# Kernel tuning notes

Measured on AMD Instinct MI355X. Metric: run time of the kernel, lower is better.

## Reference

```python
import jax, jax.numpy as jnp
import numpy as np

N_USER, N_VIDEO, N_PUB, N_TAG = 200000, 100000, 20000, 5000
EMB = 128
HALF = EMB // 2
LAYER_NUM = 3


def setup_inputs() -> dict:
    key = jax.random.key(0)
    ks = jax.random.split(key, 20)
    inp = {
        "user_emb": jax.random.normal(ks[0], (N_USER, EMB), jnp.float32),
        "video_emb": jax.random.normal(ks[1], (N_VIDEO, EMB), jnp.float32),
        "publisher_emb": jax.random.normal(ks[2], (N_PUB, EMB), jnp.float32),
        "tag_emb": jax.random.normal(ks[3], (N_TAG, EMB), jnp.float32),
    }
    # (name, E, n_src, n_dst)
    rels = [
        ("uv", 1500000, N_USER, N_VIDEO),
        ("vu", 1500000, N_VIDEO, N_USER),
        ("up", 800000, N_USER, N_PUB),
        ("pu", 800000, N_PUB, N_USER),
        ("vt", 800000, N_VIDEO, N_TAG),
        ("tv", 800000, N_TAG, N_VIDEO),
        ("pt", 400000, N_PUB, N_TAG),
        ("tp", 400000, N_TAG, N_PUB),
    ]
    for i, (name, E, ns, nd) in enumerate(rels):
        inp[name + "_src"] = jax.random.randint(ks[4 + 2 * i], (E,), 0, ns, jnp.int32)
        inp[name + "_dst"] = jax.random.randint(ks[5 + 2 * i], (E,), 0, nd, jnp.int32)
    return inp


def _seg_mean(feat, src, dst, num_dst):
    # copy_u + mean: gather half-dim src features, segment-mean onto dst.
    msg = feat[src]                                             # [E, HALF]
    s = jax.ops.segment_sum(msg, dst, num_segments=num_dst)     # [num_dst, HALF]
    deg = jax.ops.segment_sum(jnp.ones_like(dst, dtype=feat.dtype), dst,
                              num_segments=num_dst)
    return s / jnp.maximum(deg, 1.0)[:, None]  # zero-in-degree nodes -> 0 (DGL behavior)


def reference(user_emb, video_emb, publisher_emb, tag_emb,
              uv_src, uv_dst, vu_src, vu_dst,
              up_src, up_dst, pu_src, pu_dst,
              vt_src, vt_dst, tv_src, tv_dst,
              pt_src, pt_dst, tp_src, tp_dst):

    def layer(u, v, p, t):
        # user dst: [vu, pu]; video dst: [uv, tv]; publisher dst: [up, tp]; tag dst: [vt, pt]
        vu = _seg_mean(v[:, :HALF], vu_src, vu_dst, N_USER)
        pu = _seg_mean(p[:, :HALF], pu_src, pu_dst, N_USER)
        uv = _seg_mean(u[:, :HALF], uv_src, uv_dst, N_VIDEO)
        tv = _seg_mean(t[:, :HALF], tv_src, tv_dst, N_VIDEO)
        up = _seg_mean(u[:, HALF:], up_src, up_dst, N_PUB)
        tp = _seg_mean(t[:, HALF:], tp_src, tp_dst, N_PUB)
        vt = _seg_mean(v[:, HALF:], vt_src, vt_dst, N_TAG)
        pt = _seg_mean(p[:, HALF:], pt_src, pt_dst, N_TAG)
        return (jnp.concatenate([vu, pu], axis=1),
                jnp.concatenate([uv, tv], axis=1),
                jnp.concatenate([up, tp], axis=1),
                jnp.concatenate([vt, pt], axis=1))

    pu_, pv_, pp_, pt_ = user_emb, video_emb, publisher_emb, tag_emb
    u, v, p, t = user_emb, video_emb, publisher_emb, tag_emb
    for i in range(LAYER_NUM):
        u, v, p, t = layer(u, v, p, t)
        w = 1.0 / (i + 2)
        pu_ = pu_ + u * w
        pv_ = pv_ + v * w
        pp_ = pp_ + p * w
        pt_ = pt_ + t * w
    return (pu_, pv_, pp_, pt_)
```

## Files before the change

### kernel.cpp

```cpp
#include <hip/hip_runtime.h>
#include <stdint.h>

#define EMB 128
#define PCAP 12288
#define SCAP 13312

static constexpr int N_USER = 200000, N_VIDEO = 100000, N_PUB = 20000, N_TAG = 5000;
static constexpr int ROW_U = 0, ROW_V = 200000, ROW_P = 300000, ROW_T = 320000;
static constexpr int ROWS = 325000;
static constexpr int TOTAL_E = 7000000;
static constexpr int TOTAL_GROUPS = 650000;
static constexpr int TILE = 8192;
static constexpr int SORT_MAX = TOTAL_E + 7 * TOTAL_GROUPS;

using f32x4 = __attribute__((ext_vector_type(4))) float;
using u32x4 = __attribute__((ext_vector_type(4))) unsigned int;
using u32x2 = __attribute__((ext_vector_type(2))) unsigned int;

__device__ inline unsigned bf16_rne(float f) {
  unsigned u = __float_as_uint(f);
  return (u + 0x7fffu + ((u >> 16) & 1u)) >> 16;
}
__device__ inline unsigned pack_bf16x2(float lo, float hi) {
  return bf16_rne(lo) | (bf16_rne(hi) << 16);
}

__device__ inline unsigned fp8enc(float f) {
  unsigned b = __float_as_uint(f);
  unsigned s = (b >> 24) & 0x80u;
  unsigned ae = b & 0x7FFFFFFFu;
  unsigned r = ae + 0x7FFFFu + ((ae >> 20) & 1u);
  unsigned e = r >> 23;
  if (e < 121u) {
    float av = __uint_as_float(ae);
    unsigned m = (unsigned)__builtin_rintf(av * 512.0f);
    return s | m;
  }
  return s | ((e - 120u) << 3) | ((r >> 20) & 7u);
}
#if __has_builtin(__builtin_amdgcn_cvt_f32_fp8)
#define DEC4(w, x0, x1, x2, x3) \
  x0 += __builtin_amdgcn_cvt_f32_fp8((int)(w), 0); \
  x1 += __builtin_amdgcn_cvt_f32_fp8((int)(w), 1); \
  x2 += __builtin_amdgcn_cvt_f32_fp8((int)(w), 2); \
  x3 += __builtin_amdgcn_cvt_f32_fp8((int)(w), 3);
#else
__device__ inline float fp8dec(unsigned b) {
  unsigned s = (b & 0x80u) << 24;
  unsigned e = (b >> 3) & 0xFu;
  unsigned m = b & 7u;
  if (e == 0) { float f = (float)m * 0.001953125f; return s ? -f : f; }
  return __uint_as_float(s | ((e + 120u) << 23) | (m << 20));
}
#define DEC4(w, x0, x1, x2, x3) \
  x0 += fp8dec((w) & 0xffu); x1 += fp8dec(((w) >> 8) & 0xffu); \
  x2 += fp8dec(((w) >> 16) & 0xffu); x3 += fp8dec(((w) >> 24) & 0xffu);
#endif

struct SortDesc {
  int tcum[9];
  int bcum[9];
  int gcum[8];
  int E[8];
  int n_dst[8];
  int wshift[8];
  int zrow[8];
  const int* esrc[8];
  const int* edst[8];
};

struct AggrDesc {
  int cum[9];
  int src_base[8];
  int src_col[8];
  int dst_base[8];
  int dst_col[8];
  const float* demb[8];
};

__global__ __launch_bounds__(256) void part_kernel(SortDesc d, unsigned* __restrict__ pairs,
                                                   int* __restrict__ cursors) {
  __shared__ int cnt[256];
  __shared__ int lcur[256];
  int blk = blockIdx.x;
  int r = 0;
#pragma unroll
  for (int k = 1; k < 8; ++k) if (blk >= d.tcum[k]) r = k;
  int base = (blk - d.tcum[r]) * TILE;
  int n = min(TILE, d.E[r] - base);
  const int* __restrict__ esrc = d.esrc[r];
  const int* __restrict__ edst = d.edst[r];
  int tid = threadIdx.x;
  int B = d.bcum[r + 1] - d.bcum[r];
  int sh = d.wshift[r];
  int msk = (1 << sh) - 1;
  int bb = d.bcum[r];
  if (tid < B) cnt[tid] = 0;
  __syncthreads();
  for (int i = tid; i < n; i += 256)
    atomicAdd(&cnt[edst[base + i] >> sh], 1);
  __syncthreads();
  if (tid < B) {
    int c = cnt[tid];
    lcur[tid] = c ? atomicAdd(&cursors[bb + tid], c) : 0;
  }
  __syncthreads();
  for (int i = tid; i < n; i += 256) {
    int dv = edst[base + i];
    int sv = esrc[base + i];
    int b = dv >> sh;
    int pos = atomicAdd(&lcur[b], 1);
    if (pos < PCAP)
      pairs[(size_t)(bb + b) * PCAP + pos] = ((unsigned)(dv & msk) << 18) | (unsigned)sv;
  }
}

__global__ __launch_bounds__(256) void build_kernel(SortDesc d, const unsigned* __restrict__ pairs,
                                                    const int* __restrict__ cursors,
                                                    int* __restrict__ gcounter,
                                                    int* __restrict__ sorted,
                                                    int* __restrict__ Beg, int* __restrict__ Deg) {
  __shared__ int cnt[1024];
  __shared__ int poff[1025];
  __shared__ int stage[SCAP];
  __shared__ int wsums[4];
  __shared__ int sh_gbase;
  int bucket = blockIdx.x;
  int r = 0;
#pragma unroll
  for (int k = 1; k < 8; ++k) if (bucket >= d.bcum[k]) r = k;
  int bl = bucket - d.bcum[r];
  int sh = d.wshift[r];
  int first = bl << sh;
  int Wa = min(1 << sh, d.n_dst[r] - first);
  int zr = d.zrow[r];
  int tid = threadIdx.x;
  int n_b = min(cursors[bucket], PCAP);
  const unsigned* __restrict__ bp = pairs + (size_t)bucket * PCAP;

  for (int i = tid; i < 1024; i += 256) cnt[i] = 0;
  __syncthreads();
  for (int i = tid; i < n_b; i += 256)
    atomicAdd(&cnt[bp[i] >> 18], 1);
  __syncthreads();

  int t4 = tid * 4;
  int c0 = cnt[t4], c1 = cnt[t4 + 1], c2 = cnt[t4 + 2], c3 = cnt[t4 + 3];
  int p0 = (c0 + 7) & ~7, p1 = (c1 + 7) & ~7, p2 = (c2 + 7) & ~7, p3 = (c3 + 7) & ~7;
  int s = p0 + p1 + p2 + p3;
  int lane = tid & 63, wv = tid >> 6;
  int v = s;
#pragma unroll
  for (int dd = 1; dd < 64; dd <<= 1) {
    int t = __shfl_up(v, dd);
    if (lane >= dd) v += t;
  }
  if (lane == 63) wsums[wv] = v;
  __syncthreads();
  if (tid == 0) {
    int run = 0;
#pragma unroll
    for (int k = 0; k < 4; ++k) { int t = wsums[k]; wsums[k] = run; run += t; }
  }
  __syncthreads();
  int ex = wsums[wv] + (v - s);
  if (tid == 255) {
    int tot = ex + s;
    sh_gbase = atomicAdd(gcounter, tot);
    poff[1024] = min(tot, SCAP);
  }
  __syncthreads();
  int gbase = sh_gbase;
  int o0 = ex, o1 = ex + p0, o2 = o1 + p1, o3 = o2 + p2;
  cnt[t4] = o0; cnt[t4 + 1] = o1; cnt[t4 + 2] = o2; cnt[t4 + 3] = o3;
  poff[t4] = o0; poff[t4 + 1] = o1; poff[t4 + 2] = o2; poff[t4 + 3] = o3;
  int g0 = d.gcum[r] + first + t4;
  if (t4 + 0 < Wa) { Beg[g0 + 0] = gbase + o0; Deg[g0 + 0] = c0; }
  if (t4 + 1 < Wa) { Beg[g0 + 1] = gbase + o1; Deg[g0 + 1] = c1; }
  if (t4 + 2 < Wa) { Beg[g0 + 2] = gbase + o2; Deg[g0 + 2] = c2; }
  if (t4 + 3 < Wa) { Beg[g0 + 3] = gbase + o3; Deg[g0 + 3] = c3; }
  __syncthreads();

  for (int i = tid; i < n_b; i += 256) {
    unsigned pr = bp[i];
    int pos = atomicAdd(&cnt[pr >> 18], 1);
    if (pos < SCAP) stage[pos] = (int)(pr & 0x3FFFFu);
  }
  __syncthreads();
#pragma unroll
  for (int jj = 0; jj < 4; ++jj) {
    int j = t4 + jj;
    int end_ = min((j < 1023) ? poff[j + 1] : poff[1024], SCAP);
    for (int k = cnt[j]; k < end_; ++k) stage[k] = zr;
  }
  __syncthreads();

  int tot = poff[1024];
  for (int i = tid; i < tot; i += 256)
    sorted[gbase + i] = stage[i];
}

__global__ void convert_kernel(const float* __restrict__ u, const float* __restrict__ v,
                               const float* __restrict__ p, const float* __restrict__ t,
                               uint16_t* __restrict__ featA, uint16_t* __restrict__ featB,
                               unsigned char* __restrict__ f1f8) {
  int idx = blockIdx.x * blockDim.x + threadIdx.x;
  const int total8 = (ROWS + 1) * EMB / 8;
  if (idx >= total8) return;
  int flat = idx * 8;
  int row = flat >> 7;
  if (row == ROWS) {
    uint4 z = {0u, 0u, 0u, 0u};
    *(uint4*)(featA + flat) = z;
    *(uint4*)(featB + flat) = z;
    if (f1f8) { uint2 z2 = {0u, 0u}; *(uint2*)(f1f8 + flat) = z2; }
    return;
  }
  int col = flat & 127;
  const float* s;
  if (row < ROW_V)      s = u + (size_t)row * EMB + col;
  else if (row < ROW_P) s = v + (size_t)(row - ROW_V) * EMB + col;
  else if (row < ROW_T) s = p + (size_t)(row - ROW_P) * EMB + col;
  else                  s = t + (size_t)(row - ROW_T) * EMB + col;
  float4 f0 = *(const float4*)s;
  float4 f1 = *((const float4*)s + 1);
  uint4 o;
  o.x = pack_bf16x2(f0.x, f0.y);
  o.y = pack_bf16x2(f0.z, f0.w);
  o.z = pack_bf16x2(f1.x, f1.y);
  o.w = pack_bf16x2(f1.z, f1.w);
  *(uint4*)(featA + flat) = o;
}

#define ACC(q) \
  a0 += __uint_as_float((q).x << 16); a1 += __uint_as_float((q).x & 0xffff0000u); \
  a2 += __uint_as_float((q).y << 16); a3 += __uint_as_float((q).y & 0xffff0000u); \
  a4 += __uint_as_float((q).z << 16); a5 += __uint_as_float((q).z & 0xffff0000u); \
  a6 += __uint_as_float((q).w << 16); a7 += __uint_as_float((q).w & 0xffff0000u);

#define ACC8(qq) \
  DEC4((qq).x, a0, a1, a2, a3); DEC4((qq).y, a4, a5, a6, a7);

template<int M>
__global__ __launch_bounds__(256) void aggr_kernel(AggrDesc d,
    const uint16_t* __restrict__ gsrc_bf, const unsigned char* __restrict__ gsrc_f8,
    uint16_t* __restrict__ dst_bf, unsigned char* __restrict__ dst_f8,
    const uint16_t* __restrict__ f1_bf, const uint16_t* __restrict__ demb_bf,
    float* __restrict__ out,
    const int* __restrict__ sorted, const int* __restrict__ Beg,
    const int* __restrict__ Deg) {
  if ((M == 1 || M == 3) && blockIdx.x == 0 && threadIdx.x < 16) {
    uint2 z = {0u, 0u};
    *(uint2*)(dst_f8 + (size_t)ROWS * EMB + threadIdx.x * 8) = z;
  }
  int g = blockIdx.x * 32 + (threadIdx.x >> 3);
  if (g >= TOTAL_GROUPS) return;
  int lane = threadIdx.x & 7;
  int r = 0;
#pragma unroll
  for (int k = 1; k < 8; ++k) if (g >= d.cum[k]) r = k;
  int n = g - d.cum[r];
  int beg = Beg[g], dg = Deg[g];
  float recip = 1.0f / (float)(dg > 0 ? dg : 1);
  constexpr bool GB = (M == 0 || M == 3 || M == 4);
  const uint16_t* __restrict__ sb16 =
      GB ? gsrc_bf + (size_t)d.src_base[r] * EMB + d.src_col[r] + lane * 8 : nullptr;
  const unsigned char* __restrict__ sb8 =
      !GB ? gsrc_f8 + (size_t)d.src_base[r] * EMB + d.src_col[r] + lane * 8 : nullptr;
  float a0 = 0.f, a1 = 0.f, a2 = 0.f, a3 = 0.f, a4 = 0.f, a5 = 0.f, a6 = 0.f, a7 = 0.f;
  int nchunk = (dg + 7) >> 3;
  const int* ep = sorted + beg;
  int4 iA0 = {0,0,0,0}, iA1 = {0,0,0,0};
  if (nchunk > 0) { iA0 = *(const int4*)ep; iA1 = *(const int4*)(ep + 4); }
  for (int c = 0; c < nchunk; ++c) {
    int4 iB0 = {0,0,0,0}, iB1 = {0,0,0,0};
    if (c + 1 < nchunk) { iB0 = *(const int4*)(ep + 8); iB1 = *(const int4*)(ep + 12); }
    if (GB) {
      uint4 q0 = *(const uint4*)(sb16 + (size_t)iA0.x * EMB);
      uint4 q1 = *(const uint4*)(sb16 + (size_t)iA0.y * EMB);
      uint4 q2 = *(const uint4*)(sb16 + (size_t)iA0.z * EMB);
      uint4 q3 = *(const uint4*)(sb16 + (size_t)iA0.w * EMB);
      uint4 q4 = *(const uint4*)(sb16 + (size_t)iA1.x * EMB);
      uint4 q5 = *(const uint4*)(sb16 + (size_t)iA1.y * EMB);
      uint4 q6 = *(const uint4*)(sb16 + (size_t)iA1.z * EMB);
      uint4 q7 = *(const uint4*)(sb16 + (size_t)iA1.w * EMB);
      __builtin_amdgcn_sched_barrier(0);
      ACC(q0); ACC(q1); ACC(q2); ACC(q3);
      ACC(q4); ACC(q5); ACC(q6); ACC(q7);
    } else {
      uint2 q0 = *(const uint2*)(sb8 + (size_t)iA0.x * EMB);
      uint2 q1 = *(const uint2*)(sb8 + (size_t)iA0.y * EMB);
      uint2 q2 = *(const uint2*)(sb8 + (size_t)iA0.z * EMB);
      uint2 q3 = *(const uint2*)(sb8 + (size_t)iA0.w * EMB);
      uint2 q4 = *(const uint2*)(sb8 + (size_t)iA1.x * EMB);
      uint2 q5 = *(const uint2*)(sb8 + (size_t)iA1.y * EMB);
      uint2 q6 = *(const uint2*)(sb8 + (size_t)iA1.z * EMB);
      uint2 q7 = *(const uint2*)(sb8 + (size_t)iA1.w * EMB);
      __builtin_amdgcn_sched_barrier(0);
      ACC8(q0); ACC8(q1); ACC8(q2); ACC8(q3);
      ACC8(q4); ACC8(q5); ACC8(q6); ACC8(q7);
    }
    iA0 = iB0; iA1 = iB1; ep += 8;
  }
  a0 *= recip; a1 *= recip; a2 *= recip; a3 *= recip;
  a4 *= recip; a5 *= recip; a6 *= recip; a7 *= recip;

  int col = d.dst_col[r] + lane * 8;
  size_t dpos = (size_t)(d.dst_base[r] + n) * EMB + col;

  if (M == 0 || M == 4) {
    u32x4 ov;
    ov.x = pack_bf16x2(a0, a1);
    ov.y = pack_bf16x2(a2, a3);
    ov.z = pack_bf16x2(a4, a5);
    ov.w = pack_bf16x2(a6, a7);
    __builtin_nontemporal_store(ov, (u32x4*)(dst_bf + dpos));
    if (M == 4) {
      u32x2 o8;
      o8.x = fp8enc(a0) | (fp8enc(a1) << 8) | (fp8enc(a2) << 16) | (fp8enc(a3) << 24);
      o8.y = fp8enc(a4) | (fp8enc(a5) << 8) | (fp8enc(a6) << 16) | (fp8enc(a7) << 24);
      __builtin_nontemporal_store(o8, (u32x2*)(dst_f8 + dpos));
    }
    return;
  }
  if (M == 1 || M == 3) {
    u32x2 ov;
    ov.x = fp8enc(a0) | (fp8enc(a1) << 8) | (fp8enc(a2) << 16) | (fp8enc(a3) << 24);
    ov.y = fp8enc(a4) | (fp8enc(a5) << 8) | (fp8enc(a6) << 16) | (fp8enc(a7) << 24);
    __builtin_nontemporal_store(ov, (u32x2*)(dst_f8 + dpos));
    return;
  }

  u32x4 q1 = __builtin_nontemporal_load((const u32x4*)(f1_bf + dpos));
  u32x2 qf = __builtin_nontemporal_load((const u32x2*)(gsrc_f8 + dpos));
  float g0 = 0.f, g1 = 0.f, g2 = 0.f, g3 = 0.f, g4 = 0.f, g5 = 0.f, g6 = 0.f, g7 = 0.f;
  DEC4(qf.x, g0, g1, g2, g3);
  DEC4(qf.y, g4, g5, g6, g7);
  f32x4 v0, v1;
  if (demb_bf) {
    u32x4 qe = __builtin_nontemporal_load((const u32x4*)(demb_bf + dpos));
    v0.x = __uint_as_float(qe.x << 16); v0.y = __uint_as_float(qe.x & 0xffff0000u);
    v0.z = __uint_as_float(qe.y << 16); v0.w = __uint_as_float(qe.y & 0xffff0000u);
    v1.x = __uint_as_float(qe.z << 16); v1.y = __uint_as_float(qe.z & 0xffff0000u);
    v1.z = __uint_as_float(qe.w << 16); v1.w = __uint_as_float(qe.w & 0xffff0000u);
  } else {
    const f32x4* de = (const f32x4*)(d.demb[r] + (size_t)n * EMB + col);
    v0 = __builtin_nontemporal_load(de);
    v1 = __builtin_nontemporal_load(de + 1);
  }
  const float w1 = 0.5f, w2 = 1.0f / 3.0f, w3 = 0.25f;
  v0.x += w1 * __uint_as_float(q1.x << 16)         + w2 * g0 + w3 * a0;
  v0.y += w1 * __uint_as_float(q1.x & 0xffff0000u) + w2 * g1 + w3 * a1;
  v0.z += w1 * __uint_as_float(q1.y << 16)         + w2 * g2 + w3 * a2;
  v0.w += w1 * __uint_as_float(q1.y & 0xffff0000u) + w2 * g3 + w3 * a3;
  v1.x += w1 * __uint_as_float(q1.z << 16)         + w2 * g4 + w3 * a4;
  v1.y += w1 * __uint_as_float(q1.z & 0xffff0000u) + w2 * g5 + w3 * a5;
  v1.z += w1 * __uint_as_float(q1.w << 16)         + w2 * g6 + w3 * a6;
  v1.w += w1 * __uint_as_float(q1.w & 0xffff0000u) + w2 * g7 + w3 * a7;
  __builtin_nontemporal_store(v0, (f32x4*)(out + dpos));
  __builtin_nontemporal_store(v1, (f32x4*)(out + dpos) + 1);
}

extern "C" void kernel_launch(void* const* d_in, const int* in_sizes, int n_in,
                              void* d_out, int out_size, void* d_ws, size_t ws_size,
                              hipStream_t stream) {
  const float* emb_u = (const float*)d_in[0];
  const float* emb_v = (const float*)d_in[1];
  const float* emb_p = (const float*)d_in[2];
  const float* emb_t = (const float*)d_in[3];

  struct RelInfo { int si, di, E, n_dst, src_base, src_col, dst_base, dst_col, wshift; };
  const RelInfo rels[8] = {
    {12, 13,  800000, N_TAG,   ROW_V, 64, ROW_T,  0,  5},
    {16, 17,  400000, N_TAG,   ROW_P, 64, ROW_T, 64,  5},
    { 8,  9,  800000, N_PUB,   ROW_U, 64, ROW_P,  0,  7},
    {18, 19,  400000, N_PUB,   ROW_T, 64, ROW_P, 64,  7},
    { 4,  5, 1500000, N_VIDEO, ROW_U,  0, ROW_V,  0,  9},
    {14, 15,  800000, N_VIDEO, ROW_T,  0, ROW_V, 64,  9},
    { 6,  7, 1500000, N_USER,  ROW_V,  0, ROW_U,  0, 10},
    {10, 11,  800000, N_USER,  ROW_P,  0, ROW_U, 64, 10},
  };
  const float* dembs[8] = {emb_t, emb_t, emb_p, emb_p, emb_v, emb_v, emb_u, emb_u};

  char* ws = (char*)d_ws;
  size_t cursor = 0;
  auto take = [&](size_t bytes) -> char* {
    char* p = ws + cursor;
    cursor = (cursor + bytes + 255) & ~(size_t)255;
    return p;
  };
  uint16_t* featA = (uint16_t*)take((size_t)(ROWS + 1) * EMB * 2);
  uint16_t* featB = (uint16_t*)take((size_t)(ROWS + 1) * EMB * 2);
  int* sorted = (int*)take((size_t)SORT_MAX * 4);
  int* Beg    = (int*)take((size_t)TOTAL_GROUPS * 4);
  int* Deg    = (int*)take((size_t)TOTAL_GROUPS * 4);
  unsigned* pairs = (unsigned*)d_ws;

  SortDesc sd;
  AggrDesc ad;
  int tacc = 0, bacc = 0, gacc = 0;
  for (int r = 0; r < 8; ++r) {
    int n_dst = rels[r].n_dst;
    sd.tcum[r] = tacc; tacc += (rels[r].E + TILE - 1) / TILE;
    sd.bcum[r] = bacc; bacc += (n_dst + (1 << rels[r].wshift) - 1) >> rels[r].wshift;
    sd.gcum[r] = gacc;
    sd.E[r] = rels[r].E;
    sd.n_dst[r] = n_dst;
    sd.wshift[r] = rels[r].wshift;
    sd.zrow[r] = ROWS - rels[r].src_base;
    sd.esrc[r] = (const int*)d_in[rels[r].si];
    sd.edst[r] = (const int*)d_in[rels[r].di];

    ad.cum[r] = gacc;
    ad.src_base[r] = rels[r].src_base;
    ad.src_col[r] = rels[r].src_col;
    ad.dst_base[r] = rels[r].dst_base;
    ad.dst_col[r] = rels[r].dst_col;
    ad.demb[r] = dembs[r];
    gacc += n_dst;
  }
  sd.tcum[8] = tacc;
  sd.bcum[8] = bacc;
  ad.cum[8] = gacc;

  int* cursors  = (int*)take((size_t)bacc * 4 + 4);
  int* gcounter = cursors + bacc;

  const size_t f8bytes = (size_t)(ROWS + 1) * EMB;
  size_t base_need = cursor;
  unsigned char* f1fp8 = nullptr;
  unsigned char* f2fp8 = (unsigned char*)featA;
  bool use_fp8_l1 = false;
  const uint16_t* demb_bf = nullptr;
  if (ws_size >= base_need + f8bytes + 256) {
    f1fp8 = (unsigned char*)take(f8bytes);
    use_fp8_l1 = true;
    if (ws_size >= cursor + f8bytes + 256) {
      f2fp8 = (unsigned char*)take(f8bytes);
      demb_bf = featA;
    }
  }

  hipMemsetAsync(cursors, 0, (size_t)(bacc + 1) * 4, stream);
  part_kernel<<<tacc, 256, 0, stream>>>(sd, pairs, cursors);
  build_kernel<<<bacc, 256, 0, stream>>>(sd, pairs, cursors, gcounter, sorted, Beg, Deg);

  convert_kernel<<<((ROWS + 1) * EMB / 8 + 255) / 256, 256, 0, stream>>>(
      emb_u, emb_v, emb_p, emb_t, featA, featB, f1fp8);

  float* out = (float*)d_out;
  const int aggr_blocks = (TOTAL_GROUPS + 31) / 32;
  if (use_fp8_l1) {
    aggr_kernel<4><<<aggr_blocks, 256, 0, stream>>>(ad, featA, nullptr, featB, f1fp8,
                                                    nullptr, nullptr, nullptr, sorted, Beg, Deg);
    aggr_kernel<1><<<aggr_blocks, 256, 0, stream>>>(ad, nullptr, f1fp8, nullptr, f2fp8,
                                                    nullptr, nullptr, nullptr, sorted, Beg, Deg);
  } else {
    aggr_kernel<0><<<aggr_blocks, 256, 0, stream>>>(ad, featA, nullptr, featB, nullptr,
                                                    nullptr, nullptr, nullptr, sorted, Beg, Deg);
    aggr_kernel<3><<<aggr_blocks, 256, 0, stream>>>(ad, featB, nullptr, nullptr, f2fp8,
                                                    nullptr, nullptr, nullptr, sorted, Beg, Deg);
  }
  aggr_kernel<2><<<aggr_blocks, 256, 0, stream>>>(ad, nullptr, f2fp8, nullptr, nullptr,
                                                  featB, demb_bf, out, sorted, Beg, Deg);
}
```

Before: 599.6 us.

## Sub-sort edges by source tile, pad segments to 4, add 4-edge tail path

The build kernel now bins each destination's edges by source-row tile (32K rows), so the gathers for a segment walk source rows in roughly ascending order. The intent is better cache locality in the aggregation gathers. Segment padding drops from 8 to 4, which cuts the number of dummy zero-row gathers. The aggregation loop gains a 4-edge tail step and loads indices with nontemporal loads. In exchange the histogram and scan in the build kernel grow to up to 4096 bins, with a serial per-thread scan over the tiles.

```diff
diff --git a/kernel.cpp b/kernel.cpp
--- a/kernel.cpp
+++ b/kernel.cpp
@@ -4,6 +4,7 @@
 #define EMB 128
 #define PCAP 12288
 #define SCAP 13312
+#define TSHIFT 15
 
 static constexpr int N_USER = 200000, N_VIDEO = 100000, N_PUB = 20000, N_TAG = 5000;
 static constexpr int ROW_U = 0, ROW_V = 200000, ROW_P = 300000, ROW_T = 320000;
@@ -16,6 +17,7 @@
 using f32x4 = __attribute__((ext_vector_type(4))) float;
 using u32x4 = __attribute__((ext_vector_type(4))) unsigned int;
 using u32x2 = __attribute__((ext_vector_type(2))) unsigned int;
+using i32x4 = __attribute__((ext_vector_type(4))) int;
 
 __device__ inline unsigned bf16_rne(float f) {
   unsigned u = __float_as_uint(f);
@@ -64,6 +66,7 @@
   int E[8];
   int n_dst[8];
   int wshift[8];
+  int ntile[8];
   int zrow[8];
   const int* esrc[8];
   const int* edst[8];
@@ -120,34 +123,46 @@
                                                     int* __restrict__ gcounter,
                                                     int* __restrict__ sorted,
                                                     int* __restrict__ Beg, int* __restrict__ Deg) {
-  __shared__ int cnt[1024];
-  __shared__ int poff[1025];
+  __shared__ int bins[4096];
   __shared__ int stage[SCAP];
   __shared__ int wsums[4];
-  __shared__ int sh_gbase;
+  __shared__ int sh_gbase, sh_tot;
   int bucket = blockIdx.x;
   int r = 0;
 #pragma unroll
   for (int k = 1; k < 8; ++k) if (bucket >= d.bcum[k]) r = k;
   int bl = bucket - d.bcum[r];
   int sh = d.wshift[r];
+  int T = d.ntile[r];
   int first = bl << sh;
-  int Wa = min(1 << sh, d.n_dst[r] - first);
+  int W = 1 << sh;
+  int Wa = min(W, d.n_dst[r] - first);
   int zr = d.zrow[r];
   int tid = threadIdx.x;
   int n_b = min(cursors[bucket], PCAP);
   const unsigned* __restrict__ bp = pairs + (size_t)bucket * PCAP;
 
-  for (int i = tid; i < 1024; i += 256) cnt[i] = 0;
-  __syncthreads();
-  for (int i = tid; i < n_b; i += 256)
-    atomicAdd(&cnt[bp[i] >> 18], 1);
+  int NB = W * T;
+  for (int i = tid; i < NB; i += 256) bins[i] = 0;
+  __syncthreads();
+  for (int i = tid; i < n_b; i += 256) {
+    unsigned pr = bp[i];
+    atomicAdd(&bins[(int)(pr >> 18) * T + (int)((pr & 0x3FFFFu) >> TSHIFT)], 1);
+  }
   __syncthreads();
 
   int t4 = tid * 4;
-  int c0 = cnt[t4], c1 = cnt[t4 + 1], c2 = cnt[t4 + 2], c3 = cnt[t4 + 3];
-  int p0 = (c0 + 7) & ~7, p1 = (c1 + 7) & ~7, p2 = (c2 + 7) & ~7, p3 = (c3 + 7) & ~7;
-  int s = p0 + p1 + p2 + p3;
+  int c[4], p[4];
+  int s = 0;
+#pragma unroll
+  for (int jj = 0; jj < 4; ++jj) {
+    int cj = 0;
+    if (t4 + jj < W)
+      for (int t = 0; t < T; ++t) cj += bins[(t4 + jj) * T + t];
+    c[jj] = cj;
+    p[jj] = (cj + 3) & ~3;
+    s += p[jj];
+  }
   int lane = tid & 63, wv = tid >> 6;
   int v = s;
 #pragma unroll
@@ -167,35 +182,50 @@
   if (tid == 255) {
     int tot = ex + s;
     sh_gbase = atomicAdd(gcounter, tot);
-    poff[1024] = min(tot, SCAP);
+    sh_tot = min(tot, SCAP);
   }
   __syncthreads();
   int gbase = sh_gbase;
-  int o0 = ex, o1 = ex + p0, o2 = o1 + p1, o3 = o2 + p2;
-  cnt[t4] = o0; cnt[t4 + 1] = o1; cnt[t4 + 2] = o2; cnt[t4 + 3] = o3;
-  poff[t4] = o0; poff[t4 + 1] = o1; poff[t4 + 2] = o2; poff[t4 + 3] = o3;
-  int g0 = d.gcum[r] + first + t4;
-  if (t4 + 0 < Wa) { Beg[g0 + 0] = gbase + o0; Deg[g0 + 0] = c0; }
-  if (t4 + 1 < Wa) { Beg[g0 + 1] = gbase + o1; Deg[g0 + 1] = c1; }
-  if (t4 + 2 < Wa) { Beg[g0 + 2] = gbase + o2; Deg[g0 + 2] = c2; }
-  if (t4 + 3 < Wa) { Beg[g0 + 3] = gbase + o3; Deg[g0 + 3] = c3; }
+
+  int o[4];
+  {
+    int run = ex;
+#pragma unroll
+    for (int jj = 0; jj < 4; ++jj) { o[jj] = run; run += p[jj]; }
+  }
+#pragma unroll
+  for (int jj = 0; jj < 4; ++jj) {
+    int j = t4 + jj;
+    if (j < W) {
+      int run = o[jj];
+      for (int t = 0; t < T; ++t) {
+        int tmp = bins[j * T + t];
+        bins[j * T + t] = run;
+        run += tmp;
+      }
+      if (j < Wa) {
+        Beg[d.gcum[r] + first + j] = gbase + o[jj];
+        Deg[d.gcum[r] + first + j] = c[jj];
+      }
+    }
+  }
   __syncthreads();
 
   for (int i = tid; i < n_b; i += 256) {
     unsigned pr = bp[i];
-    int pos = atomicAdd(&cnt[pr >> 18], 1);
-    if (pos < SCAP) stage[pos] = (int)(pr & 0x3FFFFu);
+    int sv = (int)(pr & 0x3FFFFu);
+    int pos = atomicAdd(&bins[(int)(pr >> 18) * T + (sv >> TSHIFT)], 1);
+    if (pos < SCAP) stage[pos] = sv;
   }
   __syncthreads();
 #pragma unroll
   for (int jj = 0; jj < 4; ++jj) {
-    int j = t4 + jj;
-    int end_ = min((j < 1023) ? poff[j + 1] : poff[1024], SCAP);
-    for (int k = cnt[j]; k < end_; ++k) stage[k] = zr;
-  }
-  __syncthreads();
-
-  int tot = poff[1024];
+    int end_ = min(o[jj] + p[jj], SCAP);
+    for (int k = o[jj] + c[jj]; k < end_; ++k) stage[k] = zr;
+  }
+  __syncthreads();
+
+  int tot = sh_tot;
   for (int i = tid; i < tot; i += 256)
     sorted[gbase + i] = stage[i];
 }
@@ -268,39 +298,65 @@
   const unsigned char* __restrict__ sb8 =
       !GB ? gsrc_f8 + (size_t)d.src_base[r] * EMB + d.src_col[r] + lane * 8 : nullptr;
   float a0 = 0.f, a1 = 0.f, a2 = 0.f, a3 = 0.f, a4 = 0.f, a5 = 0.f, a6 = 0.f, a7 = 0.f;
-  int nchunk = (dg + 7) >> 3;
+  int P = (dg + 3) & ~3;
+  int n8 = P >> 3;
+  int has4 = P & 4;
   const int* ep = sorted + beg;
-  int4 iA0 = {0,0,0,0}, iA1 = {0,0,0,0};
-  if (nchunk > 0) { iA0 = *(const int4*)ep; iA1 = *(const int4*)(ep + 4); }
-  for (int c = 0; c < nchunk; ++c) {
-    int4 iB0 = {0,0,0,0}, iB1 = {0,0,0,0};
-    if (c + 1 < nchunk) { iB0 = *(const int4*)(ep + 8); iB1 = *(const int4*)(ep + 12); }
+  i32x4 iA0 = {0,0,0,0}, iA1 = {0,0,0,0};
+  if (n8 > 0) {
+    iA0 = __builtin_nontemporal_load((const i32x4*)ep);
+    iA1 = __builtin_nontemporal_load((const i32x4*)ep + 1);
+  }
+  for (int cch = 0; cch < n8; ++cch) {
+    i32x4 iB0 = {0,0,0,0}, iB1 = {0,0,0,0};
+    if (cch + 1 < n8) {
+      iB0 = __builtin_nontemporal_load((const i32x4*)(ep + 8));
+      iB1 = __builtin_nontemporal_load((const i32x4*)(ep + 8) + 1);
+    }
     if (GB) {
-      uint4 q0 = *(const uint4*)(sb16 + (size_t)iA0.x * EMB);
-      uint4 q1 = *(const uint4*)(sb16 + (size_t)iA0.y * EMB);
-      uint4 q2 = *(const uint4*)(sb16 + (size_t)iA0.z * EMB);
-      uint4 q3 = *(const uint4*)(sb16 + (size_t)iA0.w * EMB);
-      uint4 q4 = *(const uint4*)(sb16 + (size_t)iA1.x * EMB);
-      uint4 q5 = *(const uint4*)(sb16 + (size_t)iA1.y * EMB);
-      uint4 q6 = *(const uint4*)(sb16 + (size_t)iA1.z * EMB);
-      uint4 q7 = *(const uint4*)(sb16 + (size_t)iA1.w * EMB);
+      uint4 q0 = *(const uint4*)(sb16 + (size_t)iA0[0] * EMB);
+      uint4 q1 = *(const uint4*)(sb16 + (size_t)iA0[1] * EMB);
+      uint4 q2 = *(const uint4*)(sb16 + (size_t)iA0[2] * EMB);
+      uint4 q3 = *(const uint4*)(sb16 + (size_t)iA0[3] * EMB);
+      uint4 q4 = *(const uint4*)(sb16 + (size_t)iA1[0] * EMB);
+      uint4 q5 = *(const uint4*)(sb16 + (size_t)iA1[1] * EMB);
+      uint4 q6 = *(const uint4*)(sb16 + (size_t)iA1[2] * EMB);
+      uint4 q7 = *(const uint4*)(sb16 + (size_t)iA1[3] * EMB);
       __builtin_amdgcn_sched_barrier(0);
       ACC(q0); ACC(q1); ACC(q2); ACC(q3);
       ACC(q4); ACC(q5); ACC(q6); ACC(q7);
     } else {
-      uint2 q0 = *(const uint2*)(sb8 + (size_t)iA0.x * EMB);
-      uint2 q1 = *(const uint2*)(sb8 + (size_t)iA0.y * EMB);
-      uint2 q2 = *(const uint2*)(sb8 + (size_t)iA0.z * EMB);
-      uint2 q3 = *(const uint2*)(sb8 + (size_t)iA0.w * EMB);
-      uint2 q4 = *(const uint2*)(sb8 + (size_t)iA1.x * EMB);
-      uint2 q5 = *(const uint2*)(sb8 + (size_t)iA1.y * EMB);
-      uint2 q6 = *(const uint2*)(sb8 + (size_t)iA1.z * EMB);
-      uint2 q7 = *(const uint2*)(sb8 + (size_t)iA1.w * EMB);
+      uint2 q0 = *(const uint2*)(sb8 + (size_t)iA0[0] * EMB);
+      uint2 q1 = *(const uint2*)(sb8 + (size_t)iA0[1] * EMB);
+      uint2 q2 = *(const uint2*)(sb8 + (size_t)iA0[2] * EMB);
+      uint2 q3 = *(const uint2*)(sb8 + (size_t)iA0[3] * EMB);
+      uint2 q4 = *(const uint2*)(sb8 + (size_t)iA1[0] * EMB);
+      uint2 q5 = *(const uint2*)(sb8 + (size_t)iA1[1] * EMB);
+      uint2 q6 = *(const uint2*)(sb8 + (size_t)iA1[2] * EMB);
+      uint2 q7 = *(const uint2*)(sb8 + (size_t)iA1[3] * EMB);
       __builtin_amdgcn_sched_barrier(0);
       ACC8(q0); ACC8(q1); ACC8(q2); ACC8(q3);
       ACC8(q4); ACC8(q5); ACC8(q6); ACC8(q7);
     }
     iA0 = iB0; iA1 = iB1; ep += 8;
+  }
+  if (has4) {
+    i32x4 i0 = __builtin_nontemporal_load((const i32x4*)ep);
+    if (GB) {
+      uint4 q0 = *(const uint4*)(sb16 + (size_t)i0[0] * EMB);
+      uint4 q1 = *(const uint4*)(sb16 + (size_t)i0[1] * EMB);
+      uint4 q2 = *(const uint4*)(sb16 + (size_t)i0[2] * EMB);
+      uint4 q3 = *(const uint4*)(sb16 + (size_t)i0[3] * EMB);
+      __builtin_amdgcn_sched_barrier(0);
+      ACC(q0); ACC(q1); ACC(q2); ACC(q3);
+    } else {
+      uint2 q0 = *(const uint2*)(sb8 + (size_t)i0[0] * EMB);
+      uint2 q1 = *(const uint2*)(sb8 + (size_t)i0[1] * EMB);
+      uint2 q2 = *(const uint2*)(sb8 + (size_t)i0[2] * EMB);
+      uint2 q3 = *(const uint2*)(sb8 + (size_t)i0[3] * EMB);
+      __builtin_amdgcn_sched_barrier(0);
+      ACC8(q0); ACC8(q1); ACC8(q2); ACC8(q3);
+    }
   }
   a0 *= recip; a1 *= recip; a2 *= recip; a3 *= recip;
   a4 *= recip; a5 *= recip; a6 *= recip; a7 *= recip;
@@ -369,16 +425,16 @@
   const float* emb_p = (const float*)d_in[2];
   const float* emb_t = (const float*)d_in[3];
 
-  struct RelInfo { int si, di, E, n_dst, src_base, src_col, dst_base, dst_col, wshift; };
+  struct RelInfo { int si, di, E, n_dst, src_base, src_col, dst_base, dst_col, wshift, n_src; };
   const RelInfo rels[8] = {
-    {12, 13,  800000, N_TAG,   ROW_V, 64, ROW_T,  0,  5},
-    {16, 17,  400000, N_TAG,   ROW_P, 64, ROW_T, 64,  5},
-    { 8,  9,  800000, N_PUB,   ROW_U, 64, ROW_P,  0,  7},
-    {18, 19,  400000, N_PUB,   ROW_T, 64, ROW_P, 64,  7},
-    { 4,  5, 1500000, N_VIDEO, ROW_U,  0, ROW_V,  0,  9},
-    {14, 15,  800000, N_VIDEO, ROW_T,  0, ROW_V, 64,  9},
-    { 6,  7, 1500000, N_USER,  ROW_V,  0, ROW_U,  0, 10},
-    {10, 11,  800000, N_USER,  ROW_P,  0, ROW_U, 64, 10},
+    {12, 13,  800000, N_TAG,   ROW_V, 64, ROW_T,  0,  5, N_VIDEO},
+    {16, 17,  400000, N_TAG,   ROW_P, 64, ROW_T, 64,  5, N_PUB},
+    { 8,  9,  800000, N_PUB,   ROW_U, 64, ROW_P,  0,  7, N_USER},
+    {18, 19,  400000, N_PUB,   ROW_T, 64, ROW_P, 64,  7, N_TAG},
+    { 4,  5, 1500000, N_VIDEO, ROW_U,  0, ROW_V,  0,  9, N_USER},
+    {14, 15,  800000, N_VIDEO, ROW_T,  0, ROW_V, 64,  9, N_TAG},
+    { 6,  7, 1500000, N_USER,  ROW_V,  0, ROW_U,  0, 10, N_VIDEO},
+    {10, 11,  800000, N_USER,  ROW_P,  0, ROW_U, 64, 10, N_PUB},
   };
   const float* dembs[8] = {emb_t, emb_t, emb_p, emb_p, emb_v, emb_v, emb_u, emb_u};
 
@@ -407,6 +463,7 @@
     sd.E[r] = rels[r].E;
     sd.n_dst[r] = n_dst;
     sd.wshift[r] = rels[r].wshift;
+    sd.ntile[r] = (rels[r].n_src + (1 << TSHIFT) - 1) >> TSHIFT;
     sd.zrow[r] = ROWS - rels[r].src_base;
     sd.esrc[r] = (const int*)d_in[rels[r].si];
     sd.edst[r] = (const int*)d_in[rels[r].di];
```

New measurement: 633.3 us, median of 2. +5.6%, slower.
